# Kernel tuning notes

Hardware: AMD Instinct MI355X
Metric: run time of the kernel (lower is better)

The kernel has to match this reference:

```python
import jax, jax.numpy as jnp
import numpy as np

B, S, H = 2, 2048, 2048
E, K, HID = 8, 2, 4096          # num_experts, top-k, expert hidden (2*H)
NH, HD = 8, 256                  # attention heads, head_dim
MS, MD = 256, 512                # memory_size, memory_dim
RSTEPS, RD = 3, 512              # reasoning steps, reasoning_dim
SCALE = 16.0                     # sqrt(head_dim)


def setup_inputs() -> dict:
    key = jax.random.key(0)
    ks = iter(jax.random.split(key, 64))
    def w(shape, s=0.02):
        return (jax.random.normal(next(ks), shape, jnp.float32) * s)
    z = lambda *shape: jnp.zeros(shape, jnp.float32)
    inp = {
        'hidden_states': jax.random.normal(next(ks), (B, S, H), jnp.float32),
        'attention_mask': jnp.zeros((B, S), jnp.float32),  # 0 = unmasked (faithful: mask*-1e9 added)
        # MoE
        'gate_w': w((H, E)), 'gate_b': z(E),
        'moe_w1': w((E, H, HID)), 'moe_b1': z(E, HID),
        'moe_w2': w((E, HID, H)), 'moe_b2': z(E, H),
        # memory-augmented attention
        'q_w': w((H, H)), 'q_b': z(H),
        'k_w': w((H, H)), 'k_b': z(H),
        'v_w': w((H, H)), 'v_b': z(H),
        'o_w': w((H, H)), 'o_b': z(H),
        'mem_values': jax.random.normal(next(ks), (MS, MD), jnp.float32),
        'mem_proj_w': w((MD, H)), 'mem_proj_b': z(H),
        'mem_attn_w': w((H, MS)), 'mem_attn_b': z(MS),
        # hierarchical reasoning (stacked over steps)
        'rs_w1': w((RSTEPS, H, RD)), 'rs_b1': z(RSTEPS, RD),
        'rs_w2': w((RSTEPS, RD, H)), 'rs_b2': z(RSTEPS, H),
        'ln_g': jnp.ones((RSTEPS, H), jnp.float32), 'ln_b': z(RSTEPS, H),
        'hg_w1': w((RSTEPS, H, H // 4)), 'hg_b1': z(RSTEPS, H // 4),
        'hg_w2': w((RSTEPS, H // 4, 1)), 'hg_b2': z(RSTEPS, 1),
        'integ_w': w((RSTEPS * H, H)), 'integ_b': z(H),
    }
    return inp


def _layernorm(x, g, b, eps=1e-5):
    m = x.mean(-1, keepdims=True)
    v = ((x - m) ** 2).mean(-1, keepdims=True)
    return (x - m) / jnp.sqrt(v + eps) * g + b


def _forward(hidden_states, attention_mask, gate_w, gate_b, moe_w1, moe_b1, moe_w2, moe_b2,
             q_w, q_b, k_w, k_b, v_w, v_b, o_w, o_b, mem_values, mem_proj_w, mem_proj_b,
             mem_attn_w, mem_attn_b, rs_w1, rs_b1, rs_w2, rs_b2, ln_g, ln_b,
             hg_w1, hg_b1, hg_w2, hg_b2, integ_w, integ_b):
    h = hidden_states
    N = B * S
    # ---- Mixture of Experts (top-k routing, dense combine-weight formulation) ----
    x_flat = h.reshape(N, H)
    gate_probs = jax.nn.softmax(x_flat @ gate_w + gate_b, axis=-1)        # [N,E]
    topk_s, topk_i = jax.lax.top_k(gate_probs, K)                          # [N,K]
    topk_p = jax.nn.softmax(topk_s, axis=-1)                               # renormalize over top-k
    comb = jnp.zeros((N, E), x_flat.dtype).at[jnp.arange(N)[:, None], topk_i].add(topk_p)
    h1 = jax.nn.relu(jnp.einsum('nd,edh->neh', x_flat, moe_w1) + moe_b1)   # [N,E,HID]
    eo = jnp.einsum('neh,ehd->ned', h1, moe_w2) + moe_b2                   # [N,E,H]
    moe_out = jnp.einsum('ned,ne->nd', eo, comb).reshape(B, S, H)
    h = h + 0.5 * moe_out
    # ---- Memory-augmented attention ----
    q = (h @ q_w + q_b).reshape(B, S, NH, HD).transpose(0, 2, 1, 3)
    k = (h @ k_w + k_b).reshape(B, S, NH, HD).transpose(0, 2, 1, 3)
    v = (h @ v_w + v_b).reshape(B, S, NH, HD).transpose(0, 2, 1, 3)
    scores = jnp.einsum('bhqd,bhkd->bhqk', q, k) / SCALE
    scores = scores + attention_mask[:, None, None, :] * (-1e9)
    probs = jax.nn.softmax(scores, axis=-1)
    attn = jnp.einsum('bhqk,bhkd->bhqd', probs, v).transpose(0, 2, 1, 3).reshape(B, S, H)
    mem_p = jax.nn.softmax(h @ mem_attn_w + mem_attn_b, axis=-1)           # [B,S,MS]
    mem_o = (mem_p @ mem_values) @ mem_proj_w + mem_proj_b                 # [B,S,H]
    mem_out = (attn + 0.3 * mem_o) @ o_w + o_b
    h = h + mem_out
    # ---- Hierarchical reasoning ----
    cur = h
    outs = []
    for i in range(RSTEPS):
        so = jax.nn.relu(cur @ rs_w1[i] + rs_b1[i]) @ rs_w2[i] + rs_b2[i]
        so = _layernorm(so, ln_g[i], ln_b[i])
        g = jax.nn.sigmoid(jax.nn.relu(cur @ hg_w1[i] + hg_b1[i]) @ hg_w2[i] + hg_b2[i])  # [B,S,1]
        cur = cur + g * so
        outs.append(cur)
    final = jnp.concatenate(outs, axis=-1) @ integ_w + integ_b
    return h + final


def reference(hidden_states, attention_mask, gate_w, gate_b, moe_w1, moe_b1, moe_w2, moe_b2,
              q_w, q_b, k_w, k_b, v_w, v_b, o_w, o_b, mem_values, mem_proj_w, mem_proj_b,
              mem_attn_w, mem_attn_b, rs_w1, rs_b1, rs_w2, rs_b2, ln_g, ln_b,
              hg_w1, hg_b1, hg_w2, hg_b2, integ_w, integ_b):
    return _forward(hidden_states, attention_mask, gate_w, gate_b, moe_w1, moe_b1, moe_w2, moe_b2,
                    q_w, q_b, k_w, k_b, v_w, v_b, o_w, o_b, mem_values, mem_proj_w, mem_proj_b,
                    mem_attn_w, mem_attn_b, rs_w1, rs_b1, rs_w2, rs_b2, ln_g, ln_b,
                    hg_w1, hg_b1, hg_w2, hg_b2, integ_w, integ_b)
```

## Files before the change

kernel.cpp:

```cpp
#include <hip/hip_runtime.h>
#include <string.h>


typedef __attribute__((ext_vector_type(4))) float f32x4;
typedef __attribute__((ext_vector_type(8))) __bf16 bf16x8;

#define NTOK 4096
#define HDIM 2048
#define AS1 __attribute__((address_space(1)))
#define AS3 __attribute__((address_space(3)))

__device__ __forceinline__ unsigned short f2bf(float f) {
  unsigned u = __float_as_uint(f);
  unsigned r = (u + 0x7fffu + ((u >> 16) & 1u)) >> 16;
  return (unsigned short)r;
}
__device__ __forceinline__ float bf2f(unsigned short u) {
  return __uint_as_float(((unsigned)u) << 16);
}
__device__ __forceinline__ void unpack8(uint4 r, float* v) {
  v[0]=bf2f((unsigned short)(r.x&0xffff)); v[1]=bf2f((unsigned short)(r.x>>16));
  v[2]=bf2f((unsigned short)(r.y&0xffff)); v[3]=bf2f((unsigned short)(r.y>>16));
  v[4]=bf2f((unsigned short)(r.z&0xffff)); v[5]=bf2f((unsigned short)(r.z>>16));
  v[6]=bf2f((unsigned short)(r.w&0xffff)); v[7]=bf2f((unsigned short)(r.w>>16));
}
__device__ __forceinline__ uint4 pack8(const float* v) {
  uint4 r;
  r.x = (unsigned)f2bf(v[0]) | ((unsigned)f2bf(v[1])<<16);
  r.y = (unsigned)f2bf(v[2]) | ((unsigned)f2bf(v[3])<<16);
  r.z = (unsigned)f2bf(v[4]) | ((unsigned)f2bf(v[5])<<16);
  r.w = (unsigned)f2bf(v[6]) | ((unsigned)f2bf(v[7])<<16);
  return r;
}

__global__ void k_tconv(const float* __restrict__ in, unsigned short* __restrict__ out,
                        int R, int C, long inB, long outB) {
  __shared__ float tl[32][33];
  const int z = blockIdx.z;
  const float* ip = in + (long)z * inB;
  unsigned short* op = out + (long)z * outB;
  const int tx = threadIdx.x & 31, ty = threadIdx.x >> 5;
  const int c0 = blockIdx.x * 32, r0 = blockIdx.y * 32;
#pragma unroll
  for (int i = 0; i < 4; i++)
    tl[ty + i*8][tx] = ip[(long)(r0 + ty + i*8) * C + c0 + tx];
  __syncthreads();
#pragma unroll
  for (int i = 0; i < 4; i++)
    op[(long)(c0 + ty + i*8) * R + r0 + tx] = f2bf(tl[tx][ty + i*8]);
}

__global__ void k_tconv4(const float* __restrict__ i0, const float* __restrict__ i1,
                         const float* __restrict__ i2, const float* __restrict__ i3,
                         unsigned short* __restrict__ out) {
  __shared__ float tl[32][33];
  const int z = blockIdx.z;
  const float* ip = (z == 0) ? i0 : (z == 1) ? i1 : (z == 2) ? i2 : i3;
  unsigned short* op = out + (size_t)z * 2048 * 2048;
  const int tx = threadIdx.x & 31, ty = threadIdx.x >> 5;
  const int c0 = blockIdx.x * 32, r0 = blockIdx.y * 32;
#pragma unroll
  for (int i = 0; i < 4; i++)
    tl[ty + i*8][tx] = ip[(long)(r0 + ty + i*8) * 2048 + c0 + tx];
  __syncthreads();
#pragma unroll
  for (int i = 0; i < 4; i++)
    op[(long)(c0 + ty + i*8) * 2048 + r0 + tx] = f2bf(tl[tx][ty + i*8]);
}

__global__ void k_cvt(const float* __restrict__ in, unsigned short* __restrict__ out, long n4) {
  long i = (long)blockIdx.x * blockDim.x + threadIdx.x;
  if (i < n4) {
    float4 v = ((const float4*)in)[i];
    float vv[4] = {v.x, v.y, v.z, v.w};
    union { unsigned short u[4]; uint2 d; } p;
#pragma unroll
    for (int j = 0; j < 4; j++) p.u[j] = f2bf(vv[j]);
    ((uint2*)out)[i] = p.d;
  }
}

__global__ void k_tvact(const unsigned short* __restrict__ qkv, unsigned short* __restrict__ vT) {
  __shared__ unsigned short tl[32][33];
  const int z = blockIdx.z, b = z >> 3, hh = z & 7;
  const unsigned short* ip = qkv + (long)b * 2048 * 6144 + 4096 + hh * 256;
  unsigned short* op = vT + (long)z * 256 * 2048;
  const int tx = threadIdx.x & 31, ty = threadIdx.x >> 5;
  const int d0 = blockIdx.x * 32, s0 = blockIdx.y * 32;
#pragma unroll
  for (int i = 0; i < 4; i++)
    tl[ty + i*8][tx] = ip[(long)(s0 + ty + i*8) * 6144 + d0 + tx];
  __syncthreads();
#pragma unroll
  for (int i = 0; i < 4; i++)
    op[(long)(d0 + ty + i*8) * 2048 + s0 + tx] = tl[tx][ty + i*8];
}

__global__ void k_misc(const float* __restrict__ mask, float* __restrict__ mv,
                       const float* __restrict__ qb, const float* __restrict__ kb,
                       const float* __restrict__ vb, float* __restrict__ qkvb,
                       const float* __restrict__ rsb1, const float* __restrict__ hgb1,
                       float* __restrict__ rhb, int* __restrict__ meta) {
  const int b = blockIdx.x, t = threadIdx.x;
  if (b < 16) {
    int i = b * 256 + t; mv[i] = -1e9f * mask[i];
  } else if (b < 40) {
    int i = (b - 16) * 256 + t;
    qkvb[i] = (i < 2048) ? qb[i] : (i < 4096) ? kb[i - 2048] : vb[i - 4096];
  } else if (b < 46) {
    int i = (b - 40) * 256 + t;
    int s = i >> 9, c = i & 511;
    rhb[s * 1024 + c] = rsb1[i]; rhb[s * 1024 + 512 + c] = hgb1[i];
  } else {
    if (t < 8) meta[t] = 0;
  }
}

__global__ void k_gate(const float* __restrict__ x, const float* __restrict__ gw,
                       const float* __restrict__ gb, int* __restrict__ meta,
                       int* __restrict__ e0a, int* __restrict__ e1a,
                       float* __restrict__ w0a, float* __restrict__ w1a) {
  const int wv = threadIdx.x >> 6, ln = threadIdx.x & 63;
  const int n = blockIdx.x * 4 + wv;
  const float* xr = x + (long)n * HDIM;
  float s[8] = {0,0,0,0,0,0,0,0};
  for (int k = ln; k < HDIM; k += 64) {
    float xv = xr[k];
    const float* g = gw + (long)k * 8;
#pragma unroll
    for (int e = 0; e < 8; e++) s[e] += xv * g[e];
  }
#pragma unroll
  for (int e = 0; e < 8; e++)
    for (int d = 32; d; d >>= 1) s[e] += __shfl_xor(s[e], d);
  if (ln == 0) {
    float mx = -1e30f;
#pragma unroll
    for (int e = 0; e < 8; e++) { s[e] += gb[e]; mx = fmaxf(mx, s[e]); }
    float p[8], sum = 0.f;
#pragma unroll
    for (int e = 0; e < 8; e++) { p[e] = expf(s[e] - mx); sum += p[e]; }
    float inv = 1.f / sum;
#pragma unroll
    for (int e = 0; e < 8; e++) p[e] *= inv;
    int e0 = 0;
    for (int e = 1; e < 8; e++) if (p[e] > p[e0]) e0 = e;
    int e1 = (e0 == 0) ? 1 : 0;
    for (int e = 0; e < 8; e++) if (e != e0 && p[e] > p[e1]) e1 = e;
    float q = expf(p[e1] - p[e0]);
    float w0 = 1.f / (1.f + q), w1 = q / (1.f + q);
    e0a[n] = e0; e1a[n] = e1; w0a[n] = w0; w1a[n] = w1;
    atomicAdd(&meta[e0], 1); atomicAdd(&meta[e1], 1);
  }
}

__global__ void k_buildmap(int* meta) {
  if (threadIdx.x == 0 && blockIdx.x == 0) {
    int cum = 0, nT = 0;
    for (int e = 0; e < 8; e++) {
      int c = meta[e];
      meta[16 + e] = cum; meta[24 + e] = cum + c; meta[8 + e] = 0;
      int t = (c + 127) >> 7;
      for (int i = 0; i < t; i++) { meta[33 + nT] = e; meta[129 + nT] = cum + i * 128; nT++; }
      cum += c;
    }
    meta[32] = nT;
  }
}

__global__ void k_scatter(int* __restrict__ meta, const int* __restrict__ e0a,
                          const int* __restrict__ e1a, int* __restrict__ s0a,
                          int* __restrict__ s1a, int* __restrict__ srcTok) {
  const int n = blockIdx.x * 256 + threadIdx.x;
  if (n < NTOK) {
    int e0 = e0a[n], e1 = e1a[n];
    int s0 = meta[16 + e0] + atomicAdd(&meta[8 + e0], 1);
    int s1 = meta[16 + e1] + atomicAdd(&meta[8 + e1], 1);
    s0a[n] = s0; s1a[n] = s1; srcTok[s0] = n; srcTok[s1] = n;
  }
}

__global__ void k_combine(const float* __restrict__ h, const unsigned short* __restrict__ eo,
                          const int* __restrict__ s0a, const int* __restrict__ s1a,
                          const float* __restrict__ w0a, const float* __restrict__ w1a,
                          unsigned short* __restrict__ h2b) {
  const int n = blockIdx.x, c = threadIdx.x * 8;
  const float w0 = w0a[n], w1 = w1a[n];
  uint4 a = *(const uint4*)(eo + (long)s0a[n] * HDIM + c);
  uint4 b = *(const uint4*)(eo + (long)s1a[n] * HDIM + c);
  float va[8], vb[8]; unpack8(a, va); unpack8(b, vb);
  const float* hr = h + (long)n * HDIM + c;
  float o[8];
#pragma unroll
  for (int j = 0; j < 8; j++) o[j] = hr[j] + 0.5f * (w0 * va[j] + w1 * vb[j]);
  *(uint4*)(h2b + (long)n * HDIM + c) = pack8(o);
}

__global__ void k_softmax2048(unsigned short* __restrict__ p) {
  const long r = blockIdx.x;
  unsigned short* row = p + r * 2048;
  const int t = threadIdx.x, wv = t >> 6, ln = t & 63;
  uint4 raw = ((const uint4*)row)[t];
  float v[8]; unpack8(raw, v);
  float m = v[0];
#pragma unroll
  for (int j = 1; j < 8; j++) m = fmaxf(m, v[j]);
  for (int d = 32; d; d >>= 1) m = fmaxf(m, __shfl_xor(m, d));
  __shared__ float sm[4], ssum[4];
  if (ln == 0) sm[wv] = m;
  __syncthreads();
  m = fmaxf(fmaxf(sm[0], sm[1]), fmaxf(sm[2], sm[3]));
  float s = 0.f;
#pragma unroll
  for (int j = 0; j < 8; j++) { v[j] = expf(v[j] - m); s += v[j]; }
  for (int d = 32; d; d >>= 1) s += __shfl_xor(s, d);
  if (ln == 0) ssum[wv] = s;
  __syncthreads();
  s = ssum[0] + ssum[1] + ssum[2] + ssum[3];
  const float inv = 1.f / s;
#pragma unroll
  for (int j = 0; j < 8; j++) v[j] *= inv;
  ((uint4*)row)[t] = pack8(v);
}

__global__ void k_softmax256(const float* __restrict__ in, unsigned short* __restrict__ out) {
  const int wv = threadIdx.x >> 6, ln = threadIdx.x & 63;
  const long r = (long)blockIdx.x * 4 + wv;
  const float4 v4 = ((const float4*)(in + r * 256))[ln];
  float v[4] = {v4.x, v4.y, v4.z, v4.w};
  float m = fmaxf(fmaxf(v[0], v[1]), fmaxf(v[2], v[3]));
  for (int d = 32; d; d >>= 1) m = fmaxf(m, __shfl_xor(m, d));
  float s = 0.f;
#pragma unroll
  for (int j = 0; j < 4; j++) { v[j] = expf(v[j] - m); s += v[j]; }
  for (int d = 32; d; d >>= 1) s += __shfl_xor(s, d);
  const float inv = 1.f / s;
  union { unsigned short u[4]; uint2 d2; } p;
#pragma unroll
  for (int j = 0; j < 4; j++) p.u[j] = f2bf(v[j] * inv);
  ((uint2*)(out + r * 256))[ln] = p.d2;
}

__global__ void k_gdot(const unsigned short* __restrict__ g1, long ld, const float* __restrict__ w,
                       const float* __restrict__ bb, float* __restrict__ gv) {
  const int wv = threadIdx.x >> 6, ln = threadIdx.x & 63;
  const int n = blockIdx.x * 4 + wv;
  uint4 raw = *(const uint4*)(g1 + (long)n * ld + ln * 8);
  float v[8]; unpack8(raw, v);
  const float4 wa = ((const float4*)w)[ln * 2];
  const float4 wb = ((const float4*)w)[ln * 2 + 1];
  float s = v[0]*wa.x + v[1]*wa.y + v[2]*wa.z + v[3]*wa.w
          + v[4]*wb.x + v[5]*wb.y + v[6]*wb.z + v[7]*wb.w;
  for (int d = 32; d; d >>= 1) s += __shfl_xor(s, d);
  if (ln == 0) gv[n] = 1.f / (1.f + expf(-(s + bb[0])));
}

__global__ void k_lnupdate(const float* __restrict__ so, const float* __restrict__ curIn,
                           const float* __restrict__ gv, const float* __restrict__ lng,
                           const float* __restrict__ lnb, float* __restrict__ curOut,
                           unsigned short* __restrict__ curbOut, unsigned short* __restrict__ outs,
                           int step) {
  const int n = blockIdx.x, t = threadIdx.x, wv = t >> 6, ln = t & 63, c = t * 8;
  const float* row = so + (long)n * 2048 + c;
  float x[8];
#pragma unroll
  for (int j = 0; j < 8; j++) x[j] = row[j];
  float s1 = 0.f, s2 = 0.f;
#pragma unroll
  for (int j = 0; j < 8; j++) { s1 += x[j]; s2 += x[j] * x[j]; }
  for (int d = 32; d; d >>= 1) { s1 += __shfl_xor(s1, d); s2 += __shfl_xor(s2, d); }
  __shared__ float a1[4], a2[4];
  if (ln == 0) { a1[wv] = s1; a2[wv] = s2; }
  __syncthreads();
  s1 = a1[0] + a1[1] + a1[2] + a1[3];
  s2 = a2[0] + a2[1] + a2[2] + a2[3];
  const float mean = s1 * (1.f / 2048.f);
  const float var = s2 * (1.f / 2048.f) - mean * mean;
  const float rstd = rsqrtf(var + 1e-5f);
  const float g = gv[n];
  const float* ci = curIn + (long)n * 2048 + c;
  float o[8];
#pragma unroll
  for (int j = 0; j < 8; j++) {
    float l = (x[j] - mean) * rstd * lng[c + j] + lnb[c + j];
    o[j] = ci[j] + g * l;
  }
  float* co = curOut + (long)n * 2048 + c;
#pragma unroll
  for (int j = 0; j < 8; j++) co[j] = o[j];
  *(uint4*)(curbOut + (long)n * 2048 + c) = pack8(o);
  *(uint4*)(outs + (long)n * 6144 + (long)step * 2048 + c) = pack8(o);
}

struct GArgs {
  const unsigned short* A; long lda, aSO, aSI;
  const unsigned short* Bt; long ldb, bSO, bSI;
  int M, N, K;
  const float* adv; long advSO, advSI;
  float alpha, rscale;
  const float* rF; long ldrF, rfSO, rfSI;
  const unsigned short* rB; long ldrB, rbSO, rbSI;
  float* oF; long ldoF, ofSO, ofSI;
  unsigned short* oB; long ldoB, obSO, obSI;
  const int* meta;
  const int* srcTok;
};

template <int MOE, int RELU, int RESID, int OUTF, int OUTB>
__global__ __launch_bounds__(512) void gemm_bt(GArgs g) {
  __shared__ unsigned short lds[2 * 16384];
  const int t = threadIdx.x, wv = t >> 6, ln = t & 63, ln15 = ln & 15;
  const int lr8 = ln >> 3;
  const int lsl = (ln & 7) ^ lr8;
  const int bz = blockIdx.z;
  int row0, rowMax;
  const unsigned short *A, *Bt;
  long advO = 0, rFO = 0, rBO = 0, oFO = 0, oBO = 0;
  if constexpr (MOE) {
    const int ty = blockIdx.y;
    if (ty >= g.meta[32]) return;
    const int e = g.meta[33 + ty];
    row0 = g.meta[129 + ty]; rowMax = g.meta[24 + e];
    A = g.A; Bt = g.Bt + (long)e * g.bSO;
    advO = (long)e * g.advSO;
  } else {
    row0 = blockIdx.y << 7; rowMax = g.M;
    const long bo = (long)(bz >> 3), bi = (long)(bz & 7);
    A = g.A + bo * g.aSO + bi * g.aSI;
    Bt = g.Bt + bo * g.bSO + bi * g.bSI;
    advO = bo * g.advSO + bi * g.advSI;
    rFO = bo * g.rfSO + bi * g.rfSI;
    rBO = bo * g.rbSO + bi * g.rbSI;
    oFO = bo * g.ofSO + bi * g.ofSI;
    oBO = bo * g.obSO + bi * g.obSI;
  }
  const int col0 = blockIdx.x << 7;
  const long lda = g.lda, ldb = g.ldb;
  const int wm = (wv >> 2) << 6;
  const int wc = (wv & 3) << 5;

  int grow0, grow1;
  {
    int r0i = row0 + (wv << 4) + lr8;
    int r1i = r0i + 8;
    if constexpr (MOE) {
      r0i = (r0i < rowMax) ? r0i : (rowMax - 1);
      r1i = (r1i < rowMax) ? r1i : (rowMax - 1);
    }
    if constexpr (MOE == 2) { grow0 = g.srcTok[r0i]; grow1 = g.srcTok[r1i]; }
    else { grow0 = r0i; grow1 = r1i; }
  }

  auto STAGE = [&](int kt, unsigned base) {
    const long kk = ((long)kt << 6) + (lsl << 3);
    {
      const int rb = (wv << 4);
      __builtin_amdgcn_global_load_lds(
          (const AS1 void*)(A + (long)grow0 * lda + kk),
          (AS3 void*)(lds + base + (rb << 6)), 16, 0, 0);
      __builtin_amdgcn_global_load_lds(
          (const AS1 void*)(A + (long)grow1 * lda + kk),
          (AS3 void*)(lds + base + ((rb + 8) << 6)), 16, 0, 0);
    }
#pragma unroll
    for (int l = 0; l < 2; ++l) {
      const int rb = (wv << 4) + (l << 3);
      __builtin_amdgcn_global_load_lds(
          (const AS1 void*)(Bt + (long)(col0 + rb + lr8) * ldb + kk),
          (AS3 void*)(lds + base + 8192 + (rb << 6)), 16, 0, 0);
    }
  };

  const f32x4 fz = {0.f, 0.f, 0.f, 0.f};
  f32x4 acc[4][2];
#pragma unroll
  for (int i = 0; i < 4; i++)
#pragma unroll
    for (int j = 0; j < 2; j++) acc[i][j] = fz;

  const int nt = g.K >> 6;

  STAGE(0, 0);
  asm volatile("s_waitcnt vmcnt(0)" ::: "memory");
  __builtin_amdgcn_s_barrier();

  for (int kt = 0; kt < nt; ++kt) {
    const unsigned aB = (kt & 1) ? 16384u : 0u;
    const unsigned nB = aB ^ 16384u;
    if (kt + 1 < nt) STAGE(kt + 1, nB);
#pragma unroll
    for (int ks = 0; ks < 2; ++ks) {
      const int kb = (ks << 2) + (ln >> 4);
      bf16x8 bg[2];
#pragma unroll
      for (int j = 0; j < 2; ++j) {
        const int r = wc + (j << 4) + ln15;
        bg[j] = *(const bf16x8*)(lds + aB + 8192 + (r << 6) + ((kb ^ (r & 7)) << 3));
      }
      __builtin_amdgcn_s_setprio(1);
#pragma unroll
      for (int i = 0; i < 4; ++i) {
        const int r = wm + (i << 4) + ln15;
        bf16x8 a = *(const bf16x8*)(lds + aB + (r << 6) + ((kb ^ (r & 7)) << 3));
#pragma unroll
        for (int j = 0; j < 2; ++j)
          acc[i][j] = __builtin_amdgcn_mfma_f32_16x16x32_bf16(a, bg[j], acc[i][j], 0, 0, 0);
      }
      __builtin_amdgcn_s_setprio(0);
    }
    asm volatile("s_waitcnt vmcnt(0)" ::: "memory");
    __builtin_amdgcn_s_barrier();
  }

#pragma unroll
  for (int i = 0; i < 4; i++) {
#pragma unroll
    for (int j = 0; j < 2; j++) {
      const int cc = col0 + wc + (j << 4) + ln15;
      const float av = g.adv ? g.adv[advO + cc] : 0.f;
#pragma unroll
      for (int r = 0; r < 4; r++) {
        const int rr = row0 + wm + (i << 4) + ((ln >> 4) << 2) + r;
        if (rr < rowMax) {
          float v = g.alpha * acc[i][j][r] + av;
          if constexpr (RELU) v = fmaxf(v, 0.f);
          if constexpr (RESID == 1) v = g.rF[rFO + (long)rr * g.ldrF + cc] + g.rscale * v;
          if constexpr (RESID == 2) v = bf2f(g.rB[rBO + (long)rr * g.ldrB + cc]) + g.rscale * v;
          if constexpr (OUTF) g.oF[oFO + (long)rr * g.ldoF + cc] = v;
          if constexpr (OUTB) g.oB[oBO + (long)rr * g.ldoB + cc] = f2bf(v);
        }
      }
    }
  }
}

static constexpr size_t O_W1T = 0;
static constexpr size_t O_W2T = O_W1T + (size_t)8 * 4096 * 2048 * 2;
static constexpr size_t O_QT  = O_W2T + (size_t)8 * 4096 * 2048 * 2;
static constexpr size_t O_KT  = O_QT + (size_t)2048 * 2048 * 2;
static constexpr size_t O_VWT = O_KT + (size_t)2048 * 2048 * 2;
static constexpr size_t O_OT  = O_VWT + (size_t)2048 * 2048 * 2;
static constexpr size_t O_MAT = O_OT + (size_t)2048 * 2048 * 2;
static constexpr size_t O_MPT = O_MAT + (size_t)256 * 2048 * 2;
static constexpr size_t O_MVT = O_MPT + (size_t)2048 * 512 * 2;
static constexpr size_t O_RH1 = O_MVT + (size_t)512 * 256 * 2;
static constexpr size_t O_RS2 = O_RH1 + (size_t)3 * 1024 * 2048 * 2;
static constexpr size_t O_IGT = O_RS2 + (size_t)3 * 2048 * 512 * 2;
static constexpr size_t O_META= O_IGT + (size_t)2048 * 6144 * 2;
static constexpr size_t O_E0  = O_META + 4096;
static constexpr size_t O_E1  = O_E0 + 16384;
static constexpr size_t O_W0  = O_E1 + 16384;
static constexpr size_t O_W1  = O_W0 + 16384;
static constexpr size_t O_S0  = O_W1 + 16384;
static constexpr size_t O_S1  = O_S0 + 16384;
static constexpr size_t O_SRC = O_S1 + 16384;
static constexpr size_t O_MSK = O_SRC + 32768;
static constexpr size_t O_GV  = O_MSK + 16384;
static constexpr size_t O_QKVB= O_GV + 16384;
static constexpr size_t O_RHB = O_QKVB + 6144 * 4;
static constexpr size_t O_H2  = O_RHB + 3072 * 4;
static constexpr size_t O_H2B = O_H2 + (size_t)4096 * 2048 * 4;
static constexpr size_t O_H3  = O_H2B + (size_t)4096 * 2048 * 2;
static constexpr size_t O_H3B = O_H3 + (size_t)4096 * 2048 * 4;
static constexpr size_t O_ATT = O_H3B + (size_t)4096 * 2048 * 2;
static constexpr size_t O_AO2 = O_ATT + (size_t)4096 * 2048 * 2;
static constexpr size_t O_MLG = O_AO2 + (size_t)4096 * 2048 * 2;
static constexpr size_t O_MPB = O_MLG + (size_t)4096 * 256 * 4;
static constexpr size_t O_MPV = O_MPB + (size_t)4096 * 256 * 2;
static constexpr size_t O_AR  = O_MPV + (size_t)4096 * 512 * 2;
static constexpr size_t O_XB = O_AR;
static constexpr size_t O_XG = O_XB + (size_t)4096 * 2048 * 2;
static constexpr size_t O_H1 = O_XG + (size_t)8192 * 2048 * 2;
static constexpr size_t O_EO = O_H1 + (size_t)8192 * 4096 * 2;
static constexpr size_t O_QB = O_AR;
static constexpr size_t O_VT = O_QB + (size_t)3 * 4096 * 2048 * 2;
static constexpr size_t O_SC = O_VT + (size_t)4096 * 2048 * 2;
static constexpr size_t O_T1 = O_AR;
static constexpr size_t O_SOB= O_T1 + (size_t)4096 * 1024 * 2;
static constexpr size_t O_CUR= O_SOB + (size_t)4096 * 2048 * 4;
static constexpr size_t O_CRB= O_CUR + (size_t)4096 * 2048 * 4;
static constexpr size_t O_OUS= O_CRB + (size_t)4096 * 2048 * 2;

extern "C" void kernel_launch(void* const* d_in, const int* in_sizes, int n_in,
                              void* d_out, int out_size, void* d_ws, size_t ws_size,
                              hipStream_t stream) {
  (void)in_sizes; (void)n_in; (void)out_size; (void)ws_size;
  const float* h        = (const float*)d_in[0];
  const float* mask     = (const float*)d_in[1];
  const float* gate_w   = (const float*)d_in[2];
  const float* gate_b   = (const float*)d_in[3];
  const float* moe_w1   = (const float*)d_in[4];
  const float* moe_b1   = (const float*)d_in[5];
  const float* moe_w2   = (const float*)d_in[6];
  const float* moe_b2   = (const float*)d_in[7];
  const float* q_w      = (const float*)d_in[8];
  const float* q_b      = (const float*)d_in[9];
  const float* k_w      = (const float*)d_in[10];
  const float* k_b      = (const float*)d_in[11];
  const float* v_w      = (const float*)d_in[12];
  const float* v_b      = (const float*)d_in[13];
  const float* o_w      = (const float*)d_in[14];
  const float* o_b      = (const float*)d_in[15];
  const float* mem_vals = (const float*)d_in[16];
  const float* mproj_w  = (const float*)d_in[17];
  const float* mproj_b  = (const float*)d_in[18];
  const float* mattn_w  = (const float*)d_in[19];
  const float* mattn_b  = (const float*)d_in[20];
  const float* rs_w1    = (const float*)d_in[21];
  const float* rs_b1    = (const float*)d_in[22];
  const float* rs_w2    = (const float*)d_in[23];
  const float* rs_b2    = (const float*)d_in[24];
  const float* ln_g     = (const float*)d_in[25];
  const float* ln_b     = (const float*)d_in[26];
  const float* hg_w1    = (const float*)d_in[27];
  const float* hg_b1    = (const float*)d_in[28];
  const float* hg_w2    = (const float*)d_in[29];
  const float* hg_b2    = (const float*)d_in[30];
  const float* integ_w  = (const float*)d_in[31];
  const float* integ_b  = (const float*)d_in[32];

  char* ws = (char*)d_ws;
  auto U = [&](size_t o) { return (unsigned short*)(ws + o); };
  auto F = [&](size_t o) { return (float*)(ws + o); };
  auto I = [&](size_t o) { return (int*)(ws + o); };

  k_tconv<<<dim3(128, 64, 8), 256, 0, stream>>>(moe_w1, U(O_W1T), 2048, 4096, 8388608, 8388608);
  k_tconv<<<dim3(64, 128, 8), 256, 0, stream>>>(moe_w2, U(O_W2T), 4096, 2048, 8388608, 8388608);
  k_tconv4<<<dim3(64, 64, 4), 256, 0, stream>>>(q_w, k_w, v_w, o_w, U(O_QT));
  k_tconv<<<dim3(8, 64, 1), 256, 0, stream>>>(mattn_w, U(O_MAT), 2048, 256, 0, 0);
  k_tconv<<<dim3(64, 16, 1), 256, 0, stream>>>(mproj_w, U(O_MPT), 512, 2048, 0, 0);
  k_tconv<<<dim3(16, 8, 1), 256, 0, stream>>>(mem_vals, U(O_MVT), 256, 512, 0, 0);
  k_tconv<<<dim3(16, 64, 3), 256, 0, stream>>>(rs_w1, U(O_RH1), 2048, 512, 2048 * 512, 1024 * 2048);
  k_tconv<<<dim3(16, 64, 3), 256, 0, stream>>>(hg_w1, U(O_RH1) + (size_t)512 * 2048, 2048, 512,
                                               2048 * 512, 1024 * 2048);
  k_tconv<<<dim3(64, 16, 3), 256, 0, stream>>>(rs_w2, U(O_RS2), 512, 2048, 512 * 2048, 512 * 2048);
  k_tconv<<<dim3(64, 192, 1), 256, 0, stream>>>(integ_w, U(O_IGT), 6144, 2048, 0, 0);
  k_cvt<<<8192, 256, 0, stream>>>(h, U(O_XB), 2097152);
  k_misc<<<47, 256, 0, stream>>>(mask, F(O_MSK), q_b, k_b, v_b, F(O_QKVB),
                                 rs_b1, hg_b1, F(O_RHB), I(O_META));

  k_gate<<<1024, 256, 0, stream>>>(h, gate_w, gate_b, I(O_META), I(O_E0), I(O_E1), F(O_W0), F(O_W1));
  k_buildmap<<<1, 1, 0, stream>>>(I(O_META));
  k_scatter<<<16, 256, 0, stream>>>(I(O_META), I(O_E0), I(O_E1), I(O_S0), I(O_S1), I(O_SRC));

  GArgs z0; memset(&z0, 0, sizeof(z0)); z0.alpha = 1.f; z0.rscale = 1.f;
  {
    GArgs g = z0;
    g.A = U(O_XB); g.lda = 2048;
    g.Bt = U(O_W1T); g.ldb = 2048; g.bSO = (long)4096 * 2048;
    g.N = 4096; g.K = 2048;
    g.adv = moe_b1; g.advSO = 4096;
    g.oB = U(O_H1); g.ldoB = 4096;
    g.meta = I(O_META); g.srcTok = I(O_SRC);
    gemm_bt<2, 1, 0, 0, 1><<<dim3(32, 72, 1), 512, 0, stream>>>(g);
  }
  {
    GArgs g = z0;
    g.A = U(O_H1); g.lda = 4096;
    g.Bt = U(O_W2T); g.ldb = 4096; g.bSO = (long)2048 * 4096;
    g.N = 2048; g.K = 4096;
    g.adv = moe_b2; g.advSO = 2048;
    g.oB = U(O_EO); g.ldoB = 2048;
    g.meta = I(O_META);
    gemm_bt<1, 0, 0, 0, 1><<<dim3(16, 72, 1), 512, 0, stream>>>(g);
  }
  k_combine<<<4096, 256, 0, stream>>>(h, U(O_EO), I(O_S0), I(O_S1), F(O_W0), F(O_W1), U(O_H2B));

  {
    GArgs g = z0;
    g.A = U(O_H2B); g.lda = 2048; g.M = 4096; g.N = 6144; g.K = 2048;
    g.Bt = U(O_QT); g.ldb = 2048;
    g.adv = F(O_QKVB);
    g.oB = U(O_QB); g.ldoB = 6144;
    gemm_bt<0, 0, 0, 0, 1><<<dim3(48, 32, 1), 512, 0, stream>>>(g);
  }
  k_tvact<<<dim3(8, 64, 16), 256, 0, stream>>>(U(O_QB), U(O_VT));
  {
    GArgs g = z0;
    g.A = U(O_QB); g.lda = 6144; g.aSO = 12582912; g.aSI = 256;
    g.Bt = U(O_QB) + 2048; g.ldb = 6144; g.bSO = 12582912; g.bSI = 256;
    g.M = 2048; g.N = 2048; g.K = 256;
    g.adv = F(O_MSK); g.advSO = 2048; g.advSI = 0;
    g.alpha = 0.0625f;
    g.oB = U(O_SC); g.ldoB = 2048; g.obSO = 33554432; g.obSI = 4194304;
    gemm_bt<0, 0, 0, 0, 1><<<dim3(16, 16, 16), 512, 0, stream>>>(g);
  }
  k_softmax2048<<<32768, 256, 0, stream>>>(U(O_SC));
  {
    GArgs g = z0;
    g.A = U(O_SC); g.lda = 2048; g.aSO = 33554432; g.aSI = 4194304;
    g.Bt = U(O_VT); g.ldb = 2048; g.bSO = 4194304; g.bSI = 524288;
    g.M = 2048; g.N = 256; g.K = 2048;
    g.oB = U(O_ATT); g.ldoB = 2048; g.obSO = 4194304; g.obSI = 256;
    gemm_bt<0, 0, 0, 0, 1><<<dim3(2, 16, 16), 512, 0, stream>>>(g);
  }
  {
    GArgs g = z0;
    g.A = U(O_H2B); g.lda = 2048; g.Bt = U(O_MAT); g.ldb = 2048;
    g.M = 4096; g.N = 256; g.K = 2048;
    g.adv = mattn_b;
    g.oF = F(O_MLG); g.ldoF = 256;
    gemm_bt<0, 0, 0, 1, 0><<<dim3(2, 32, 1), 512, 0, stream>>>(g);
  }
  k_softmax256<<<1024, 256, 0, stream>>>(F(O_MLG), U(O_MPB));
  {
    GArgs g = z0;
    g.A = U(O_MPB); g.lda = 256; g.Bt = U(O_MVT); g.ldb = 256;
    g.M = 4096; g.N = 512; g.K = 256;
    g.oB = U(O_MPV); g.ldoB = 512;
    gemm_bt<0, 0, 0, 0, 1><<<dim3(4, 32, 1), 512, 0, stream>>>(g);
  }
  {
    GArgs g = z0;
    g.A = U(O_MPV); g.lda = 512; g.Bt = U(O_MPT); g.ldb = 512;
    g.M = 4096; g.N = 2048; g.K = 512;
    g.adv = mproj_b;
    g.rB = U(O_ATT); g.ldrB = 2048; g.rscale = 0.3f;
    g.oB = U(O_AO2); g.ldoB = 2048;
    gemm_bt<0, 0, 2, 0, 1><<<dim3(16, 32, 1), 512, 0, stream>>>(g);
  }
  {
    GArgs g = z0;
    g.A = U(O_AO2); g.lda = 2048; g.Bt = U(O_OT); g.ldb = 2048;
    g.M = 4096; g.N = 2048; g.K = 2048;
    g.adv = o_b;
    g.rB = U(O_H2B); g.ldrB = 2048; g.rscale = 1.f;
    g.oF = F(O_H3); g.ldoF = 2048;
    g.oB = U(O_H3B); g.ldoB = 2048;
    gemm_bt<0, 0, 2, 1, 1><<<dim3(16, 32, 1), 512, 0, stream>>>(g);
  }

  for (int i = 0; i < 3; i++) {
    const unsigned short* curb = (i == 0) ? U(O_H3B) : U(O_CRB);
    const float* curf = (i == 0) ? F(O_H3) : F(O_CUR);
    {
      GArgs g = z0;
      g.A = curb; g.lda = 2048;
      g.Bt = U(O_RH1) + (size_t)i * 1024 * 2048; g.ldb = 2048;
      g.M = 4096; g.N = 1024; g.K = 2048;
      g.adv = F(O_RHB) + i * 1024;
      g.oB = U(O_T1); g.ldoB = 1024;
      gemm_bt<0, 1, 0, 0, 1><<<dim3(8, 32, 1), 512, 0, stream>>>(g);
    }
    {
      GArgs g = z0;
      g.A = U(O_T1); g.lda = 1024;
      g.Bt = U(O_RS2) + (size_t)i * 2048 * 512; g.ldb = 512;
      g.M = 4096; g.N = 2048; g.K = 512;
      g.adv = rs_b2 + i * 2048;
      g.oF = F(O_SOB); g.ldoF = 2048;
      gemm_bt<0, 0, 0, 1, 0><<<dim3(16, 32, 1), 512, 0, stream>>>(g);
    }
    k_gdot<<<1024, 256, 0, stream>>>(U(O_T1) + 512, 1024, hg_w2 + i * 512, hg_b2 + i, F(O_GV));
    k_lnupdate<<<4096, 256, 0, stream>>>(F(O_SOB), curf, F(O_GV), ln_g + i * 2048,
                                         ln_b + i * 2048, F(O_CUR), U(O_CRB), U(O_OUS), i);
  }
  {
    GArgs g = z0;
    g.A = U(O_OUS); g.lda = 6144; g.Bt = U(O_IGT); g.ldb = 6144;
    g.M = 4096; g.N = 2048; g.K = 6144;
    g.adv = integ_b;
    g.rF = F(O_H3); g.ldrF = 2048; g.rscale = 1.f;
    g.oF = (float*)d_out; g.ldoF = 2048;
    gemm_bt<0, 0, 1, 1, 0><<<dim3(16, 32, 1), 512, 0, stream>>>(g);
  }
}
```

Measured before the change: 1.663 ms.

## Fuse attention softmax into the P·V matmul kernel

Replaces the standalone row softmax over the bf16 score matrix and the generic P·V GEMM with one kernel. Each block first makes a pass over its 64 score rows to compute the row max and sum. It then recomputes the normalized probabilities on the fly while loading the A tiles, and feeds them to MFMA against V tiles staged with global_load_lds. This removes the write-back of the normalized probability matrix and one kernel launch. In exchange the scores are read twice, the exponentials are recomputed, and the grid is small (512 blocks, each with a serial 32-step K loop and no double buffering).

```diff
diff --git a/kernel.cpp b/kernel.cpp
--- a/kernel.cpp
+++ b/kernel.cpp
@@ -194,33 +194,6 @@
 #pragma unroll
   for (int j = 0; j < 8; j++) o[j] = hr[j] + 0.5f * (w0 * va[j] + w1 * vb[j]);
   *(uint4*)(h2b + (long)n * HDIM + c) = pack8(o);
-}
-
-__global__ void k_softmax2048(unsigned short* __restrict__ p) {
-  const long r = blockIdx.x;
-  unsigned short* row = p + r * 2048;
-  const int t = threadIdx.x, wv = t >> 6, ln = t & 63;
-  uint4 raw = ((const uint4*)row)[t];
-  float v[8]; unpack8(raw, v);
-  float m = v[0];
-#pragma unroll
-  for (int j = 1; j < 8; j++) m = fmaxf(m, v[j]);
-  for (int d = 32; d; d >>= 1) m = fmaxf(m, __shfl_xor(m, d));
-  __shared__ float sm[4], ssum[4];
-  if (ln == 0) sm[wv] = m;
-  __syncthreads();
-  m = fmaxf(fmaxf(sm[0], sm[1]), fmaxf(sm[2], sm[3]));
-  float s = 0.f;
-#pragma unroll
-  for (int j = 0; j < 8; j++) { v[j] = expf(v[j] - m); s += v[j]; }
-  for (int d = 32; d; d >>= 1) s += __shfl_xor(s, d);
-  if (ln == 0) ssum[wv] = s;
-  __syncthreads();
-  s = ssum[0] + ssum[1] + ssum[2] + ssum[3];
-  const float inv = 1.f / s;
-#pragma unroll
-  for (int j = 0; j < 8; j++) v[j] *= inv;
-  ((uint4*)row)[t] = pack8(v);
 }
 
 __global__ void k_softmax256(const float* __restrict__ in, unsigned short* __restrict__ out) {
@@ -429,6 +402,118 @@
           if constexpr (OUTF) g.oF[oFO + (long)rr * g.ldoF + cc] = v;
           if constexpr (OUTB) g.oB[oBO + (long)rr * g.ldoB + cc] = f2bf(v);
         }
+      }
+    }
+  }
+}
+
+__global__ __launch_bounds__(512) void k_pv(const unsigned short* __restrict__ S,
+                                            const unsigned short* __restrict__ Vt,
+                                            unsigned short* __restrict__ O) {
+  __shared__ unsigned short lds[4096 + 16384];
+  __shared__ float pm[64][8], ps[64][8];
+  __shared__ float smax[64], sinv[64];
+  const int t = threadIdx.x, wv = t >> 6, ln = t & 63, ln15 = ln & 15;
+  const int lr8 = ln >> 3, lk = ln & 7;
+  const int lsl = lk ^ lr8;
+  const int rt = blockIdx.x, bh = blockIdx.y;
+  const int b = bh >> 3, hh = bh & 7;
+  const int row0 = rt << 6;
+  const unsigned short* Sb = S + (long)bh * 2048 * 2048;
+  const unsigned short* Vb = Vt + (long)bh * 256 * 2048;
+
+  {
+    const int r = t >> 3, sg = t & 7;
+    const unsigned short* p = Sb + (long)(row0 + r) * 2048 + sg * 256;
+    float m = -3.0e38f, s = 0.f;
+    for (int i = 0; i < 32; ++i) {
+      uint4 raw = ((const uint4*)p)[i];
+      float v[8]; unpack8(raw, v);
+      float m8 = v[0];
+#pragma unroll
+      for (int j = 1; j < 8; j++) m8 = fmaxf(m8, v[j]);
+      const float mn = fmaxf(m, m8);
+      s *= expf(m - mn);
+#pragma unroll
+      for (int j = 0; j < 8; j++) s += expf(v[j] - mn);
+      m = mn;
+    }
+    pm[r][sg] = m; ps[r][sg] = s;
+  }
+  __syncthreads();
+  if (t < 64) {
+    float m = pm[t][0];
+#pragma unroll
+    for (int j = 1; j < 8; j++) m = fmaxf(m, pm[t][j]);
+    float s = 0.f;
+#pragma unroll
+    for (int j = 0; j < 8; j++) s += ps[t][j] * expf(pm[t][j] - m);
+    smax[t] = m; sinv[t] = 1.f / s;
+  }
+  __syncthreads();
+  const int arow = (wv << 3) + lr8;
+  const float am = smax[arow], ainv = sinv[arow];
+
+  const f32x4 fz = {0.f, 0.f, 0.f, 0.f};
+  f32x4 acc[4][2];
+#pragma unroll
+  for (int i = 0; i < 4; i++)
+#pragma unroll
+    for (int j = 0; j < 2; j++) acc[i][j] = fz;
+
+  const int wc = wv << 5;
+
+  for (int kt = 0; kt < 32; ++kt) {
+    const long kk = ((long)kt << 6) + (lsl << 3);
+    const uint4 araw = *(const uint4*)(Sb + (long)(row0 + arow) * 2048 + kk);
+#pragma unroll
+    for (int l = 0; l < 4; ++l) {
+      const int rb = (l << 6) + (wv << 3);
+      __builtin_amdgcn_global_load_lds(
+          (const AS1 void*)(Vb + (long)(rb + lr8) * 2048 + kk),
+          (AS3 void*)(lds + 4096 + (rb << 6)), 16, 0, 0);
+    }
+    {
+      float v[8]; unpack8(araw, v);
+      float pvv[8];
+#pragma unroll
+      for (int j = 0; j < 8; j++) pvv[j] = expf(v[j] - am) * ainv;
+      *(uint4*)(lds + (arow << 6) + (lk << 3)) = pack8(pvv);
+    }
+    __syncthreads();
+#pragma unroll
+    for (int ks = 0; ks < 2; ++ks) {
+      const int kb = (ks << 2) + (ln >> 4);
+      bf16x8 bg[2];
+#pragma unroll
+      for (int j = 0; j < 2; ++j) {
+        const int r = wc + (j << 4) + ln15;
+        bg[j] = *(const bf16x8*)(lds + 4096 + (r << 6) + ((kb ^ (r & 7)) << 3));
+      }
+      __builtin_amdgcn_s_setprio(1);
+#pragma unroll
+      for (int i = 0; i < 4; ++i) {
+        const int r = (i << 4) + ln15;
+        bf16x8 a = *(const bf16x8*)(lds + (r << 6) + ((kb ^ (r & 7)) << 3));
+#pragma unroll
+        for (int j = 0; j < 2; ++j)
+          acc[i][j] = __builtin_amdgcn_mfma_f32_16x16x32_bf16(a, bg[j], acc[i][j], 0, 0, 0);
+      }
+      __builtin_amdgcn_s_setprio(0);
+    }
+    __syncthreads();
+  }
+
+  unsigned short* Ob = O + (long)b * 2048 * 2048 + hh * 256;
+#pragma unroll
+  for (int i = 0; i < 4; ++i) {
+#pragma unroll
+    for (int j = 0; j < 2; ++j) {
+      const int cc = wc + (j << 4) + ln15;
+#pragma unroll
+      for (int r = 0; r < 4; ++r) {
+        const int rr = row0 + (i << 4) + ((ln >> 4) << 2) + r;
+        Ob[(long)rr * 2048 + cc] = f2bf(acc[i][j][r]);
       }
     }
   }
@@ -585,15 +670,7 @@
     g.oB = U(O_SC); g.ldoB = 2048; g.obSO = 33554432; g.obSI = 4194304;
     gemm_bt<0, 0, 0, 0, 1><<<dim3(16, 16, 16), 512, 0, stream>>>(g);
   }
-  k_softmax2048<<<32768, 256, 0, stream>>>(U(O_SC));
-  {
-    GArgs g = z0;
-    g.A = U(O_SC); g.lda = 2048; g.aSO = 33554432; g.aSI = 4194304;
-    g.Bt = U(O_VT); g.ldb = 2048; g.bSO = 4194304; g.bSI = 524288;
-    g.M = 2048; g.N = 256; g.K = 2048;
-    g.oB = U(O_ATT); g.ldoB = 2048; g.obSO = 4194304; g.obSI = 256;
-    gemm_bt<0, 0, 0, 0, 1><<<dim3(2, 16, 16), 512, 0, stream>>>(g);
-  }
+  k_pv<<<dim3(32, 16, 1), 512, 0, stream>>>(U(O_SC), U(O_VT), U(O_ATT));
   {
     GArgs g = z0;
     g.A = U(O_H2B); g.lda = 2048; g.Bt = U(O_MAT); g.ldb = 2048;
```

Measured after the change: 1.677 ms. No clear change (+0.9%).
